# Optimization experiments

Hardware: AMD Instinct MI355X
Metric: run time of the kernel (lower is better)

The kernel has to match this reference:

```python
import jax, jax.numpy as jnp
import numpy as np

N = 100000      # nodes
E = 1600000     # edges (avg degree 16)
IN, H, H4, OUT = 2, 128, 32, 64
B = 1000        # batch_size for final view


def setup_inputs() -> dict:
    key = jax.random.key(0)
    ks = jax.random.split(key, 16)
    w = lambda k, s: (jax.random.normal(k, s, jnp.float32) * (1.0 / np.sqrt(s[0])))
    return {
        "x": jax.random.normal(ks[0], (N, IN), jnp.float32),
        "edge_index": jax.random.randint(ks[1], (2, E), 0, N, dtype=jnp.int32),
        "batch_size": B,
        "W1": w(ks[2], (IN, H)),  "b1": jnp.zeros((H,), jnp.float32),
        "W2": w(ks[3], (H, H)),   "b2": jnp.zeros((H,), jnp.float32),
        "W3": w(ks[4], (H, H4)),  "b3": jnp.zeros((H4,), jnp.float32),
        "W4": w(ks[5], (H4, H4)), "b4": jnp.zeros((H4,), jnp.float32),
        "W5": w(ks[6], (H4, OUT)),"b5": jnp.zeros((OUT,), jnp.float32),
        "Wl": w(ks[7], (OUT, 1)), "bl": jnp.zeros((1,), jnp.float32),
    }


def gcn_conv(x, src, dst, W, b, n):
    # PyG GCNConv: add self-loops, symmetric degree normalization, scatter-add.
    h = x @ W  # [N, F]
    deg = jax.ops.segment_sum(jnp.ones(src.shape[0], h.dtype), dst,
                              num_segments=n) + 1.0  # +1 for self-loop
    dinv = jax.lax.rsqrt(deg)  # deg >= 1, no inf
    norm = dinv[src] * dinv[dst]  # [E]
    agg = jax.ops.segment_sum(h[src] * norm[:, None], dst, num_segments=n)
    agg = agg + h * (dinv * dinv)[:, None]  # self-loop contribution
    return agg + b


def reference(x, edge_index, batch_size, W1, b1, W2, b2, W3, b3, W4, b4, W5, b5, Wl, bl):
    x = x.reshape(-1, 2)
    n = x.shape[0]
    src, dst = edge_index[0], edge_index[1]
    for W, b in ((W1, b1), (W2, b2), (W3, b3), (W4, b4), (W5, b5)):
        x = jax.nn.relu(gcn_conv(x, src, dst, W, b, n))
    x = x @ Wl + bl  # [N, 1]
    return x.reshape(batch_size, -1)
```

## Files before the change

### kernel.cpp

```cpp
#include <hip/hip_runtime.h>
#include <math.h>


static inline int cdiv(int a, int b) { return (a + b - 1) / b; }

__global__ void zero_i32(int* __restrict__ p, int n) {
    int i = blockIdx.x * 256 + threadIdx.x;
    if (i < n) p[i] = 0;
}

__global__ void count_kernel(const int* __restrict__ dst, int* __restrict__ cnt, int E) {
    int e = blockIdx.x * 256 + threadIdx.x;
    if (e < E) atomicAdd(&cnt[dst[e]], 1);
}

__global__ void scan1(const int* __restrict__ cnt, int* __restrict__ off,
                      int* __restrict__ bsum, int n) {
    __shared__ int sm[256];
    int i = blockIdx.x * 256 + threadIdx.x;
    int v = (i < n) ? cnt[i] : 0;
    sm[threadIdx.x] = v;
    __syncthreads();
    for (int ofs = 1; ofs < 256; ofs <<= 1) {
        int t = (threadIdx.x >= (unsigned)ofs) ? sm[threadIdx.x - ofs] : 0;
        __syncthreads();
        sm[threadIdx.x] += t;
        __syncthreads();
    }
    if (i < n) off[i] = sm[threadIdx.x];
    if (threadIdx.x == 255) bsum[blockIdx.x] = sm[255];
}

__global__ void scan2(const int* __restrict__ bsum, int* __restrict__ bpre,
                      int nb, int* __restrict__ off, int N, int E) {
    __shared__ int sm[512];
    int t = threadIdx.x;
    sm[t] = (t < nb) ? bsum[t] : 0;
    __syncthreads();
    for (int ofs = 1; ofs < 512; ofs <<= 1) {
        int v = (t >= ofs) ? sm[t - ofs] : 0;
        __syncthreads();
        sm[t] += v;
        __syncthreads();
    }
    if (t < nb) bpre[t] = sm[t] - bsum[t];
    if (t == 0) off[N] = E;
}

__global__ void scan3(const int* __restrict__ cnt, const int* __restrict__ bpre,
                      int* __restrict__ off, int* __restrict__ cursor, int n) {
    int i = blockIdx.x * 256 + threadIdx.x;
    if (i < n) {
        off[i] = off[i] - cnt[i] + bpre[blockIdx.x];
        cursor[i] = 0;
    }
}

__global__ void dinv_xs_kernel(const int* __restrict__ cnt, const float* __restrict__ x,
                               float* __restrict__ dinv, float* __restrict__ xs, int n) {
    int i = blockIdx.x * 256 + threadIdx.x;
    if (i < n) {
        float dv = 1.0f / sqrtf((float)cnt[i] + 1.0f);
        dinv[i] = dv;
        float2 xv = *reinterpret_cast<const float2*>(x + 2 * (size_t)i);
        *reinterpret_cast<float2*>(xs + 2 * (size_t)i) = float2{dv * xv.x, dv * xv.y};
    }
}

__global__ void fill_kernel(const int* __restrict__ src, const int* __restrict__ dst,
                            const int* __restrict__ off, int* __restrict__ cursor,
                            int* __restrict__ csr, int E) {
    int e = blockIdx.x * 256 + threadIdx.x;
    if (e < E) {
        int d = dst[e];
        int p = atomicAdd(&cursor[d], 1);
        csr[off[d] + p] = src[e];
    }
}

__global__ __launch_bounds__(256) void agg2_kernel(const float* __restrict__ xs,
                                                   const int* __restrict__ off,
                                                   const int* __restrict__ csr,
                                                   const float* __restrict__ dinv,
                                                   float* __restrict__ out, int n) {
    int v = blockIdx.x * 256 + threadIdx.x;
    if (v >= n) return;
    float a0 = 0.f, a1 = 0.f;
    int e0 = off[v], e1 = off[v + 1];
    for (int e = e0; e < e1; e++) {
        int s = csr[e];
        float2 q = *reinterpret_cast<const float2*>(xs + 2 * (size_t)s);
        a0 += q.x;
        a1 += q.y;
    }
    float dv = dinv[v];
    float2 xv = *reinterpret_cast<const float2*>(xs + 2 * (size_t)v);
    *reinterpret_cast<float2*>(out + 2 * (size_t)v) =
        float2{dv * (a0 + xv.x), dv * (a1 + xv.y)};
}

template <int F, int L, bool BR, bool PS>
__global__ __launch_bounds__(256) void agg_kernel(const float* __restrict__ h,
                                                  const int* __restrict__ off,
                                                  const int* __restrict__ csr,
                                                  const float* __restrict__ dinv,
                                                  const float* __restrict__ bias,
                                                  float* __restrict__ out, int n) {
    static_assert(F == 4 * L, "each lane owns 4 cols");
    constexpr int NPW = 64 / L;
    constexpr int NPB = 4 * NPW;

    int tid = threadIdx.x;
    int wave = tid >> 6;
    int lane = tid & 63;
    int sub = lane / L;
    int sl = lane % L;
    int v = blockIdx.x * NPB + wave * NPW + sub;
    if (v >= n) return;

    int start = off[v];
    int end = off[v + 1];
    int subbase = sub * L;

    float a0 = 0.f, a1 = 0.f, a2 = 0.f, a3 = 0.f;

    for (int base = start; base < end; base += L) {
        int m = end - base;
        if (m > L) m = L;
        int idx = (sl < m) ? csr[base + sl] : 0;
        int i = 0;
        for (; i + 1 < m; i += 2) {
            int s0 = __shfl(idx, subbase + i);
            int s1 = __shfl(idx, subbase + i + 1);
            float4 h0 = *reinterpret_cast<const float4*>(h + (size_t)s0 * F + sl * 4);
            float4 h1 = *reinterpret_cast<const float4*>(h + (size_t)s1 * F + sl * 4);
            a0 += h0.x + h1.x;
            a1 += h0.y + h1.y;
            a2 += h0.z + h1.z;
            a3 += h0.w + h1.w;
        }
        if (i < m) {
            int s0 = __shfl(idx, subbase + i);
            float4 h0 = *reinterpret_cast<const float4*>(h + (size_t)s0 * F + sl * 4);
            a0 += h0.x;
            a1 += h0.y;
            a2 += h0.z;
            a3 += h0.w;
        }
    }

    float dv = dinv[v];
    float4 hv = *reinterpret_cast<const float4*>(h + (size_t)v * F + sl * 4);
    float o0 = dv * (a0 + hv.x);
    float o1 = dv * (a1 + hv.y);
    float o2 = dv * (a2 + hv.z);
    float o3 = dv * (a3 + hv.w);
    if constexpr (BR) {
        float4 b = *reinterpret_cast<const float4*>(bias + sl * 4);
        o0 = fmaxf(o0 + b.x, 0.f);
        o1 = fmaxf(o1 + b.y, 0.f);
        o2 = fmaxf(o2 + b.z, 0.f);
        o3 = fmaxf(o3 + b.w, 0.f);
    }
    if constexpr (PS) {
        o0 *= dv; o1 *= dv; o2 *= dv; o3 *= dv;
    }
    *reinterpret_cast<float4*>(out + (size_t)v * F + sl * 4) = float4{o0, o1, o2, o3};
}

template <int K, int F, bool BR, bool PS>
__global__ __launch_bounds__(256, 4) void gemm_tiled(const float* __restrict__ x,
                                                     const float* __restrict__ W,
                                                     const float* __restrict__ bias,
                                                     const float* __restrict__ dinv,
                                                     float* __restrict__ h, int n) {
    constexpr int KC = 16;
    constexpr int KCP = 20;
    constexpr int ROWS = 64;
    constexpr int TPC = F / 4;
    constexpr int RT = 256 / TPC;
    constexpr int RPT = ROWS / RT;
    static_assert(K % KC == 0, "K must be a multiple of 16");

    __shared__ float Ws[KC * F];
    __shared__ float Xs[ROWS * KCP];

    const int tid = threadIdx.x;
    const int cb = (tid % TPC) * 4;
    const int tr = tid / TPC;
    const int row0 = blockIdx.x * ROWS;

    float acc[RPT][4];
#pragma unroll
    for (int r = 0; r < RPT; r++)
#pragma unroll
        for (int j = 0; j < 4; j++) acc[r][j] = 0.f;

#pragma unroll 1
    for (int k0 = 0; k0 < K; k0 += KC) {
        __syncthreads();
        {
            int r = tid >> 2;
            int kk = (tid & 3) * 4;
            int gr = row0 + r;
            float4 v = (gr < n)
                ? *reinterpret_cast<const float4*>(x + (size_t)gr * K + k0 + kk)
                : float4{0.f, 0.f, 0.f, 0.f};
            *reinterpret_cast<float4*>(&Xs[r * KCP + kk]) = v;
        }
        for (int i = tid; i < KC * F / 4; i += 256) {
            *reinterpret_cast<float4*>(&Ws[i * 4]) =
                *reinterpret_cast<const float4*>(W + (size_t)k0 * F + i * 4);
        }
        __syncthreads();

#pragma unroll
        for (int kk4 = 0; kk4 < KC; kk4 += 4) {
            float4 xr[RPT];
#pragma unroll
            for (int r = 0; r < RPT; r++)
                xr[r] = *reinterpret_cast<const float4*>(&Xs[(tr * RPT + r) * KCP + kk4]);
#pragma unroll
            for (int j = 0; j < 4; j++) {
                float4 w = *reinterpret_cast<const float4*>(&Ws[(kk4 + j) * F + cb]);
#pragma unroll
                for (int r = 0; r < RPT; r++) {
                    float xv = (j == 0) ? xr[r].x : (j == 1) ? xr[r].y
                             : (j == 2) ? xr[r].z : xr[r].w;
                    acc[r][0] += xv * w.x;
                    acc[r][1] += xv * w.y;
                    acc[r][2] += xv * w.z;
                    acc[r][3] += xv * w.w;
                }
            }
        }
    }

    float4 b = float4{0.f, 0.f, 0.f, 0.f};
    if constexpr (BR) b = *reinterpret_cast<const float4*>(bias + cb);
#pragma unroll
    for (int r = 0; r < RPT; r++) {
        int row = row0 + tr * RPT + r;
        if (row < n) {
            float o0 = acc[r][0], o1 = acc[r][1], o2 = acc[r][2], o3 = acc[r][3];
            if constexpr (BR) {
                o0 = fmaxf(o0 + b.x, 0.f);
                o1 = fmaxf(o1 + b.y, 0.f);
                o2 = fmaxf(o2 + b.z, 0.f);
                o3 = fmaxf(o3 + b.w, 0.f);
            }
            if constexpr (PS) {
                float dv = dinv[row];
                o0 *= dv; o1 *= dv; o2 *= dv; o3 *= dv;
            }
            *reinterpret_cast<float4*>(&h[(size_t)row * F + cb]) = float4{o0, o1, o2, o3};
        }
    }
}

template <int K, int F, bool BR, bool PS>
__global__ __launch_bounds__(256, 4) void gemm_small(const float* __restrict__ x,
                                                     const float* __restrict__ W,
                                                     const float* __restrict__ bias,
                                                     const float* __restrict__ dinv,
                                                     float* __restrict__ h, int n) {
    constexpr int TPR = F / 4;
    constexpr int ROWS = 256 / TPR;
    __shared__ float Ws[K * F];
    for (int i = threadIdx.x; i < K * F; i += 256) Ws[i] = W[i];
    __syncthreads();

    int tid = threadIdx.x;
    int cb = (tid % TPR) * 4;
    int r = blockIdx.x * ROWS + tid / TPR;
    if (r >= n) return;

    const float* xr = x + (size_t)r * K;
    float a0 = 0.f, a1 = 0.f, a2 = 0.f, a3 = 0.f;
#pragma unroll
    for (int k = 0; k < K; k++) {
        float xv = xr[k];
        float4 w = *reinterpret_cast<const float4*>(&Ws[k * F + cb]);
        a0 += xv * w.x; a1 += xv * w.y; a2 += xv * w.z; a3 += xv * w.w;
    }
    if constexpr (BR) {
        float4 b = *reinterpret_cast<const float4*>(bias + cb);
        a0 = fmaxf(a0 + b.x, 0.f);
        a1 = fmaxf(a1 + b.y, 0.f);
        a2 = fmaxf(a2 + b.z, 0.f);
        a3 = fmaxf(a3 + b.w, 0.f);
    }
    if constexpr (PS) {
        float dv = dinv[r];
        a0 *= dv; a1 *= dv; a2 *= dv; a3 *= dv;
    }
    *reinterpret_cast<float4*>(&h[(size_t)r * F + cb]) = float4{a0, a1, a2, a3};
}

__global__ __launch_bounds__(256) void final_kernel(const float* __restrict__ x,
                                                    const float* __restrict__ Wl,
                                                    const float* __restrict__ bl,
                                                    float* __restrict__ out, int n) {
    __shared__ float w[64];
    if (threadIdx.x < 64) w[threadIdx.x] = Wl[threadIdx.x];
    __syncthreads();
    int i = blockIdx.x * 256 + threadIdx.x;
    if (i >= n) return;
    const float* r = x + (size_t)i * 64;
    float acc = 0.f;
#pragma unroll
    for (int k = 0; k < 64; k += 4) {
        float4 xv = *reinterpret_cast<const float4*>(r + k);
        acc += xv.x * w[k] + xv.y * w[k + 1] + xv.z * w[k + 2] + xv.w * w[k + 3];
    }
    out[i] = acc + bl[0];
}

extern "C" void kernel_launch(void* const* d_in, const int* in_sizes, int n_in,
                              void* d_out, int out_size, void* d_ws, size_t ws_size,
                              hipStream_t stream) {
    const float* x = (const float*)d_in[0];
    const int* ei = (const int*)d_in[1];
    const float* W1 = (const float*)d_in[3];
    const float* b1 = (const float*)d_in[4];
    const float* W2 = (const float*)d_in[5];
    const float* b2 = (const float*)d_in[6];
    const float* W3 = (const float*)d_in[7];
    const float* b3 = (const float*)d_in[8];
    const float* W4 = (const float*)d_in[9];
    const float* b4 = (const float*)d_in[10];
    const float* W5 = (const float*)d_in[11];
    const float* b5 = (const float*)d_in[12];
    const float* Wl = (const float*)d_in[13];
    const float* bl = (const float*)d_in[14];

    const int N = in_sizes[0] / 2;
    const int E = in_sizes[1] / 2;
    const int* src = ei;
    const int* dst = ei + E;

    char* wp = (char*)d_ws;
    auto alloc = [&](size_t bytes) -> void* {
        void* p = wp;
        wp += ((bytes + 255) / 256) * 256;
        return p;
    };
    int* cnt = (int*)alloc((size_t)N * 4);
    int* off = (int*)alloc((size_t)(N + 1) * 4);
    int* cursor = (int*)alloc((size_t)N * 4);
    int* bsum = (int*)alloc(512 * 4);
    int* bpre = (int*)alloc(512 * 4);
    int* csr = (int*)alloc((size_t)E * 4);
    float* dinv = (float*)alloc((size_t)N * 4);
    float* xs2 = (float*)alloc((size_t)N * 2 * 4);
    float* t2 = (float*)alloc((size_t)N * 2 * 4);
    float* bufA = (float*)alloc((size_t)N * 128 * 4);
    float* bufB = (float*)alloc((size_t)N * 128 * 4);

    const int gE = cdiv(E, 256);
    const int gN = cdiv(N, 256);
    const int nb = gN;
    const int gT = cdiv(N, 64);

    zero_i32<<<gN, 256, 0, stream>>>(cnt, N);
    count_kernel<<<gE, 256, 0, stream>>>(dst, cnt, E);
    scan1<<<nb, 256, 0, stream>>>(cnt, off, bsum, N);
    scan2<<<1, 512, 0, stream>>>(bsum, bpre, nb, off, N, E);
    scan3<<<nb, 256, 0, stream>>>(cnt, bpre, off, cursor, N);
    dinv_xs_kernel<<<gN, 256, 0, stream>>>(cnt, x, dinv, xs2, N);
    fill_kernel<<<gE, 256, 0, stream>>>(src, dst, off, cursor, csr, E);

    agg2_kernel<<<gN, 256, 0, stream>>>(xs2, off, csr, dinv, t2, N);
    gemm_small<2, 128, true, true><<<cdiv(N, 8), 256, 0, stream>>>(t2, W1, b1, dinv, bufA, N);
    gemm_tiled<128, 128, false, false><<<gT, 256, 0, stream>>>(bufA, W2, nullptr, nullptr, bufB, N);
    agg_kernel<128, 32, true, true><<<cdiv(N, 8), 256, 0, stream>>>(bufB, off, csr, dinv, b2, bufA, N);
    gemm_tiled<128, 32, false, false><<<gT, 256, 0, stream>>>(bufA, W3, nullptr, nullptr, bufB, N);
    agg_kernel<32, 8, true, true><<<cdiv(N, 32), 256, 0, stream>>>(bufB, off, csr, dinv, b3, bufA, N);
    gemm_tiled<32, 32, false, false><<<gT, 256, 0, stream>>>(bufA, W4, nullptr, nullptr, bufB, N);
    agg_kernel<32, 8, true, true><<<cdiv(N, 32), 256, 0, stream>>>(bufB, off, csr, dinv, b4, bufA, N);
    agg_kernel<32, 8, false, false><<<cdiv(N, 32), 256, 0, stream>>>(bufA, off, csr, dinv, nullptr, bufB, N);
    gemm_tiled<32, 64, true, false><<<gT, 256, 0, stream>>>(bufB, W5, b5, nullptr, bufA, N);
    final_kernel<<<gN, 256, 0, stream>>>(bufA, Wl, bl, (float*)d_out, N);
}
```

Baseline: 589.7 us.

## Vectorize CSR build atomics, fuse scan3 with dinv, unroll aggregation gathers

```diff
diff --git a/kernel.cpp b/kernel.cpp
--- a/kernel.cpp
+++ b/kernel.cpp
@@ -9,9 +9,20 @@
     if (i < n) p[i] = 0;
 }
 
-__global__ void count_kernel(const int* __restrict__ dst, int* __restrict__ cnt, int E) {
-    int e = blockIdx.x * 256 + threadIdx.x;
-    if (e < E) atomicAdd(&cnt[dst[e]], 1);
+__global__ __launch_bounds__(256) void count_kernel(const int* __restrict__ dst,
+                                                    int* __restrict__ cnt, int E) {
+    int q = blockIdx.x * 256 + threadIdx.x;
+    int nq = E >> 2;
+    if (q < nq) {
+        int4 d = reinterpret_cast<const int4*>(dst)[q];
+        atomicAdd(&cnt[d.x], 1);
+        atomicAdd(&cnt[d.y], 1);
+        atomicAdd(&cnt[d.z], 1);
+        atomicAdd(&cnt[d.w], 1);
+    }
+    if (q == 0) {
+        for (int e = nq * 4; e < E; e++) atomicAdd(&cnt[dst[e]], 1);
+    }
 }
 
 __global__ void scan1(const int* __restrict__ cnt, int* __restrict__ off,
@@ -47,34 +58,46 @@
     if (t == 0) off[N] = E;
 }
 
-__global__ void scan3(const int* __restrict__ cnt, const int* __restrict__ bpre,
-                      int* __restrict__ off, int* __restrict__ cursor, int n) {
+__global__ void scan3_fused(const int* __restrict__ cnt, const int* __restrict__ bpre,
+                            int* __restrict__ off, int* __restrict__ cursor,
+                            const float* __restrict__ x, float* __restrict__ dinv,
+                            float* __restrict__ xs, int n) {
     int i = blockIdx.x * 256 + threadIdx.x;
     if (i < n) {
-        off[i] = off[i] - cnt[i] + bpre[blockIdx.x];
-        cursor[i] = 0;
-    }
-}
-
-__global__ void dinv_xs_kernel(const int* __restrict__ cnt, const float* __restrict__ x,
-                               float* __restrict__ dinv, float* __restrict__ xs, int n) {
-    int i = blockIdx.x * 256 + threadIdx.x;
-    if (i < n) {
-        float dv = 1.0f / sqrtf((float)cnt[i] + 1.0f);
+        int c = cnt[i];
+        int o = off[i] - c + bpre[blockIdx.x];
+        off[i] = o;
+        cursor[i] = o;
+        float dv = 1.0f / sqrtf((float)c + 1.0f);
         dinv[i] = dv;
         float2 xv = *reinterpret_cast<const float2*>(x + 2 * (size_t)i);
         *reinterpret_cast<float2*>(xs + 2 * (size_t)i) = float2{dv * xv.x, dv * xv.y};
     }
 }
 
-__global__ void fill_kernel(const int* __restrict__ src, const int* __restrict__ dst,
-                            const int* __restrict__ off, int* __restrict__ cursor,
-                            int* __restrict__ csr, int E) {
-    int e = blockIdx.x * 256 + threadIdx.x;
-    if (e < E) {
-        int d = dst[e];
-        int p = atomicAdd(&cursor[d], 1);
-        csr[off[d] + p] = src[e];
+__global__ __launch_bounds__(256) void fill_kernel(const int* __restrict__ src,
+                                                   const int* __restrict__ dst,
+                                                   int* __restrict__ cursor,
+                                                   int* __restrict__ csr, int E) {
+    int q = blockIdx.x * 256 + threadIdx.x;
+    int nq = E >> 2;
+    if (q < nq) {
+        int4 d = reinterpret_cast<const int4*>(dst)[q];
+        int4 s = reinterpret_cast<const int4*>(src)[q];
+        int p0 = atomicAdd(&cursor[d.x], 1);
+        int p1 = atomicAdd(&cursor[d.y], 1);
+        int p2 = atomicAdd(&cursor[d.z], 1);
+        int p3 = atomicAdd(&cursor[d.w], 1);
+        __builtin_nontemporal_store(s.x, &csr[p0]);
+        __builtin_nontemporal_store(s.y, &csr[p1]);
+        __builtin_nontemporal_store(s.z, &csr[p2]);
+        __builtin_nontemporal_store(s.w, &csr[p3]);
+    }
+    if (q == 0) {
+        for (int e = nq * 4; e < E; e++) {
+            int p = atomicAdd(&cursor[dst[e]], 1);
+            csr[p] = src[e];
+        }
     }
 }
 
@@ -129,23 +152,44 @@
         if (m > L) m = L;
         int idx = (sl < m) ? csr[base + sl] : 0;
         int i = 0;
-        for (; i + 1 < m; i += 2) {
+        for (; i + 8 <= m; i += 8) {
+            float4 hb[8];
+#pragma unroll
+            for (int u = 0; u < 8; u++) {
+                int s = __shfl(idx, subbase + i + u);
+                hb[u] = *reinterpret_cast<const float4*>(h + (size_t)s * F + sl * 4);
+            }
+#pragma unroll
+            for (int u = 0; u < 8; u++) {
+                a0 += hb[u].x; a1 += hb[u].y; a2 += hb[u].z; a3 += hb[u].w;
+            }
+        }
+        if (i + 4 <= m) {
+            float4 hb[4];
+#pragma unroll
+            for (int u = 0; u < 4; u++) {
+                int s = __shfl(idx, subbase + i + u);
+                hb[u] = *reinterpret_cast<const float4*>(h + (size_t)s * F + sl * 4);
+            }
+#pragma unroll
+            for (int u = 0; u < 4; u++) {
+                a0 += hb[u].x; a1 += hb[u].y; a2 += hb[u].z; a3 += hb[u].w;
+            }
+            i += 4;
+        }
+        if (i + 2 <= m) {
             int s0 = __shfl(idx, subbase + i);
             int s1 = __shfl(idx, subbase + i + 1);
             float4 h0 = *reinterpret_cast<const float4*>(h + (size_t)s0 * F + sl * 4);
             float4 h1 = *reinterpret_cast<const float4*>(h + (size_t)s1 * F + sl * 4);
-            a0 += h0.x + h1.x;
-            a1 += h0.y + h1.y;
-            a2 += h0.z + h1.z;
-            a3 += h0.w + h1.w;
+            a0 += h0.x + h1.x; a1 += h0.y + h1.y;
+            a2 += h0.z + h1.z; a3 += h0.w + h1.w;
+            i += 2;
         }
         if (i < m) {
             int s0 = __shfl(idx, subbase + i);
             float4 h0 = *reinterpret_cast<const float4*>(h + (size_t)s0 * F + sl * 4);
-            a0 += h0.x;
-            a1 += h0.y;
-            a2 += h0.z;
-            a3 += h0.w;
+            a0 += h0.x; a1 += h0.y; a2 += h0.z; a3 += h0.w;
         }
     }
 
@@ -357,18 +401,17 @@
     float* bufA = (float*)alloc((size_t)N * 128 * 4);
     float* bufB = (float*)alloc((size_t)N * 128 * 4);
 
-    const int gE = cdiv(E, 256);
     const int gN = cdiv(N, 256);
+    const int gE4 = cdiv(cdiv(E, 4), 256);
     const int nb = gN;
     const int gT = cdiv(N, 64);
 
     zero_i32<<<gN, 256, 0, stream>>>(cnt, N);
-    count_kernel<<<gE, 256, 0, stream>>>(dst, cnt, E);
+    count_kernel<<<gE4, 256, 0, stream>>>(dst, cnt, E);
     scan1<<<nb, 256, 0, stream>>>(cnt, off, bsum, N);
     scan2<<<1, 512, 0, stream>>>(bsum, bpre, nb, off, N, E);
-    scan3<<<nb, 256, 0, stream>>>(cnt, bpre, off, cursor, N);
-    dinv_xs_kernel<<<gN, 256, 0, stream>>>(cnt, x, dinv, xs2, N);
-    fill_kernel<<<gE, 256, 0, stream>>>(src, dst, off, cursor, csr, E);
+    scan3_fused<<<nb, 256, 0, stream>>>(cnt, bpre, off, cursor, x, dinv, xs2, N);
+    fill_kernel<<<gE4, 256, 0, stream>>>(src, dst, cursor, csr, E);
 
     agg2_kernel<<<gN, 256, 0, stream>>>(xs2, off, csr, dinv, t2, N);
     gemm_small<2, 128, true, true><<<cdiv(N, 8), 256, 0, stream>>>(t2, W1, b1, dinv, bufA, N);
```

Measured after the change: 642.5 us. 1.09x slower.
